# Kernel tuning notes

Measured on AMD Instinct MI355X. Metric: run time of the kernel, lower is better.

## Reference

```python
import jax, jax.numpy as jnp
import numpy as np

B, T, I, H, N, M, O = 256, 128, 512, 512, 1024, 512, 512
EPS = 1e-8


def setup_inputs() -> dict:
    key = jax.random.key(0)
    ks = jax.random.split(key, 10)
    rn = lambda k, shape, s: jax.random.normal(k, shape, jnp.float32) * s
    s_h, s_i, s_m = 1.0 / np.sqrt(H), 1.0 / np.sqrt(I), 1.0 / np.sqrt(M)
    return {
        "x": jax.random.normal(ks[0], (B, T, 1, I), jnp.float32),
        "mem0": jnp.full((N, M), 1e-6, jnp.float32),          # memory init fill_(1e-6)
        "wr0": jnp.eye(B, N, dtype=jnp.float32),               # torch.eye(batch, N)
        "ww0": jnp.eye(B, N, dtype=jnp.float32),
        "h0": rn(ks[1], (B, H), 1.0 / H),                      # normal_(0, 1/num_hidden)
        "Wx": rn(ks[2], (I, H), s_i),
        "Wr": rn(ks[3], (M, H), s_m),
        "bh": jnp.zeros((H,), jnp.float32),
        "Whr": rn(ks[4], (H, M + 6), s_h),                      # read head: k,beta,g,s(3),gamma
        "bhr": jnp.zeros((M + 6,), jnp.float32),
        "Whw": rn(ks[5], (H, M + 6), s_h),                      # write head addressing
        "bhw": jnp.zeros((M + 6,), jnp.float32),
        "Wea": rn(ks[6], (H, 2 * M), s_h),                      # write head erase/add
        "bea": jnp.zeros((2 * M,), jnp.float32),
        "Wo": rn(ks[7], (H, O), s_h),
        "bo": jnp.zeros((O,), jnp.float32),
    }


def _address(h, w_prev, mem, Wh, bh_):
    # Standard NTM addressing: content -> interpolate -> shift -> sharpen.
    p = h @ Wh + bh_                                   # (B, M+6)
    k = jnp.tanh(p[:, :M])                             # key (B, M)
    beta = jax.nn.softplus(p[:, M:M + 1])              # strength >= 0
    g = jax.nn.sigmoid(p[:, M + 1:M + 2])              # gate in (0,1)
    s = jax.nn.softmax(p[:, M + 2:M + 5], axis=-1)     # shift over {-1,0,+1}
    gamma = 1.0 + jax.nn.softplus(p[:, M + 5:M + 6])   # sharpen >= 1
    kn = k / (jnp.linalg.norm(k, axis=-1, keepdims=True) + EPS)
    mn = mem / (jnp.linalg.norm(mem, axis=-1, keepdims=True) + EPS)
    wc = jax.nn.softmax(beta * (kn @ mn.T), axis=-1)   # content weights (B, N)
    wg = g * wc + (1.0 - g) * w_prev                   # interpolation (strictly > 0)
    wt = (s[:, 0:1] * jnp.roll(wg, -1, axis=1)
          + s[:, 1:2] * wg
          + s[:, 2:3] * jnp.roll(wg, 1, axis=1))       # circular shift conv
    wp = wt ** gamma
    return wp / (jnp.sum(wp, axis=-1, keepdims=True) + EPS)


def reference(x, mem0, wr0, ww0, h0, Wx, Wr, bh, Whr, bhr, Whw, bhw, Wea, bea, Wo, bo):
    xs = jnp.transpose(x[:, :, 0, :], (1, 0, 2))       # (T, B, I): x.permute(1,0,2,3)

    def step(carry, x_t):
        mem, wr, ww, h = carry
        # write head (get_weights=False): erase/add into memory with prev ww
        ea = h @ Wea + bea
        e = jax.nn.sigmoid(ea[:, :M])                  # (B, M)
        a = jnp.tanh(ea[:, M:])                        # (B, M)
        mem = (mem * (1.0 - jnp.einsum('bn,bm->nm', ww, e) / B)
               + jnp.einsum('bn,bm->nm', ww, a) / B)   # batch-averaged, mem shared (N, M)
        # read head (get_weights=False): r = wr @ M
        r = wr @ mem                                   # (B, M)
        # controller.step(x_t, r)
        h = jnp.tanh(x_t @ Wx + r @ Wr + bh)           # (B, H)
        # new addressing weights from updated hidden + updated memory
        ww = _address(h, ww, mem, Whw, bhw)
        wr = _address(h, wr, mem, Whr, bhr)
        out = jax.nn.sigmoid(h @ Wo + bo)              # (B, O)
        return (mem, wr, ww, h), out

    _, outs = jax.lax.scan(step, (mem0, wr0, ww0, h0), xs)  # outs (T, B, O)
    return jnp.transpose(outs, (1, 0, 2))              # (B, T, O)
```

## Files before the change

kernel.cpp:

```cpp
#include <hip/hip_runtime.h>
#include <math.h>

#define B_ 256
#define T_ 128
#define I_ 512
#define H_ 512
#define N_ 1024
#define M_ 512
#define O_ 512
#define EPS_ 1e-8f
#define NB_ 512

typedef unsigned short u16;
typedef unsigned long long u64;
typedef __attribute__((ext_vector_type(8))) short v8s;
typedef __attribute__((ext_vector_type(4))) float v4f;

#define MFMA(a, b, c) __builtin_amdgcn_mfma_f32_16x16x32_bf16(a, b, c, 0, 0, 0)

#define PL_BIG 1310720
#define PL_WXT 262144
#define PL_WRT 262144
#define PL_MEM 524288
#define PL_W   262144
#define PL_H   131072
#define PL_KH  262144

template <typename T>
__device__ __forceinline__ T lda_(const T* p) {
    return __hip_atomic_load(const_cast<T*>(p), __ATOMIC_RELAXED, __HIP_MEMORY_SCOPE_AGENT);
}
template <typename T>
__device__ __forceinline__ void sta_(T* p, T v) {
    __hip_atomic_store(p, v, __ATOMIC_RELAXED, __HIP_MEMORY_SCOPE_AGENT);
}
__device__ __forceinline__ uint4 ld16_(const u16* p) {
    const u64* q = (const u64*)p;
    u64 lo = __hip_atomic_load(const_cast<u64*>(q), __ATOMIC_RELAXED, __HIP_MEMORY_SCOPE_AGENT);
    u64 hi = __hip_atomic_load(const_cast<u64*>(q + 1), __ATOMIC_RELAXED, __HIP_MEMORY_SCOPE_AGENT);
    uint4 r;
    r.x = (unsigned)lo; r.y = (unsigned)(lo >> 32);
    r.z = (unsigned)hi; r.w = (unsigned)(hi >> 32);
    return r;
}
__device__ __forceinline__ void st64_(u16* p, u16 a, u16 b, u16 c, u16 d) {
    u64 v = (u64)a | ((u64)b << 16) | ((u64)c << 32) | ((u64)d << 48);
    __hip_atomic_store((u64*)p, v, __ATOMIC_RELAXED, __HIP_MEMORY_SCOPE_AGENT);
}

__device__ __forceinline__ float sigm_(float x) { return 1.f / (1.f + expf(-x)); }
__device__ __forceinline__ float softplus_(float x) { return x > 20.f ? x : log1pf(expf(x)); }
__device__ __forceinline__ u16 f2bf(float f) {
    unsigned u = __float_as_uint(f);
    u += 0x7fffu + ((u >> 16) & 1u);
    return (u16)(u >> 16);
}
__device__ __forceinline__ float bf2f(u16 h) { return __uint_as_float((unsigned)h << 16); }
__device__ __forceinline__ void split2(float f, u16& h, u16& m) {
    h = f2bf(f);
    m = f2bf(f - bf2f(h));
}

__device__ __forceinline__ float wave_sum_(float v) {
#pragma unroll
    for (int o = 32; o > 0; o >>= 1) v += __shfl_down(v, o);
    return v;
}
__device__ __forceinline__ float wave_max_(float v) {
#pragma unroll
    for (int o = 32; o > 0; o >>= 1) v = fmaxf(v, __shfl_down(v, o));
    return v;
}
__device__ float block_sum_(float v, float* s) {
    int lane = threadIdx.x & 63, wid = threadIdx.x >> 6, nw = blockDim.x >> 6;
    v = wave_sum_(v);
    if (lane == 0) s[wid] = v;
    __syncthreads();
    float r = (threadIdx.x < nw) ? s[threadIdx.x] : 0.f;
    if (wid == 0) { r = wave_sum_(r); if (lane == 0) s[0] = r; }
    __syncthreads();
    float out = s[0];
    __syncthreads();
    return out;
}
__device__ float block_max_(float v, float* s) {
    int lane = threadIdx.x & 63, wid = threadIdx.x >> 6, nw = blockDim.x >> 6;
    v = wave_max_(v);
    if (lane == 0) s[wid] = v;
    __syncthreads();
    float r = (threadIdx.x < nw) ? s[threadIdx.x] : -3.4e38f;
    if (wid == 0) { r = wave_max_(r); if (lane == 0) s[0] = r; }
    __syncthreads();
    float out = s[0];
    __syncthreads();
    return out;
}

__device__ __forceinline__ void gsync(unsigned* slots, unsigned* flag, unsigned epoch) {
    __syncthreads();
    if (threadIdx.x == 0)
        __hip_atomic_store(&slots[blockIdx.x * 16], epoch, __ATOMIC_RELAXED,
                           __HIP_MEMORY_SCOPE_AGENT);
    if (blockIdx.x == 0) {
        while (__hip_atomic_load(&slots[threadIdx.x * 16], __ATOMIC_RELAXED,
                                 __HIP_MEMORY_SCOPE_AGENT) < epoch)
            __builtin_amdgcn_s_sleep(1);
        while (__hip_atomic_load(&slots[(threadIdx.x + 256) * 16], __ATOMIC_RELAXED,
                                 __HIP_MEMORY_SCOPE_AGENT) < epoch)
            __builtin_amdgcn_s_sleep(1);
        __syncthreads();
        if (threadIdx.x == 0)
            __hip_atomic_store(flag, epoch, __ATOMIC_RELAXED, __HIP_MEMORY_SCOPE_AGENT);
    } else if (threadIdx.x == 0) {
        while (__hip_atomic_load(flag, __ATOMIC_RELAXED, __HIP_MEMORY_SCOPE_AGENT) < epoch)
            __builtin_amdgcn_s_sleep(1);
    }
    __syncthreads();
}

struct EpiEA0 {
    const float* bea; u16* eT; u16* aT;
    __device__ void operator()(int r0, int c, v4f v) const {
#pragma unroll
        for (int r = 0; r < 4; r++) {
            float val = v[r] + bea[c];
            u16* dst;
            int b = r0 + r;
            if (c < M_) { val = sigm_(val); dst = eT + (size_t)c * B_ + b; }
            else        { val = tanhf(val); dst = aT + (size_t)(c - M_) * B_ + b; }
            u16 h, m; split2(val, h, m);
            dst[0] = h; dst[PL_H] = m;
        }
    }
};
struct EpiR {
    u16* rp;
    __device__ void operator()(int r0, int c, v4f v) const {
#pragma unroll
        for (int r = 0; r < 4; r++) {
            u16 h, m; split2(v[r], h, m);
            size_t idx = (size_t)(r0 + r) * M_ + c;
            sta_(rp + idx, h); sta_(rp + PL_H + idx, m);
        }
    }
};
struct EpiH {
    const float* xwxt; const float* bh; float* hf; u16* hp;
    __device__ void operator()(int r0, int c, v4f v) const {
#pragma unroll
        for (int r = 0; r < 4; r++) {
            int b = r0 + r;
            float val = tanhf(v[r] + xwxt[(size_t)b * (T_ * O_) + c] + bh[c]);
            size_t idx = (size_t)b * H_ + c;
            sta_(hf + idx, val);
            u16 h, m; split2(val, h, m);
            sta_(hp + idx, h); sta_(hp + PL_H + idx, m);
        }
    }
};
struct EpiFused {
    const float* bhw; const float* bhr; const float* bo; const float* bea;
    u16* khp; float* outt; u16* eT; u16* aT;
    __device__ void operator()(int r0, int c, v4f v) const {
        if (c < 1024) {
            int head = c >> 9, key = c & 511;
            const float* bb = head ? bhr : bhw;
#pragma unroll
            for (int r = 0; r < 4; r++) {
                float val = tanhf(v[r] + bb[key]);
                size_t idx = (size_t)(head * 256 + r0 + r) * M_ + key;
                u16 h, m; split2(val, h, m);
                sta_(khp + idx, h); sta_(khp + PL_KH + idx, m);
            }
        } else if (c < 1536) {
            int o = c - 1024;
#pragma unroll
            for (int r = 0; r < 4; r++)
                outt[(size_t)(r0 + r) * (T_ * O_) + o] = sigm_(v[r] + bo[o]);
        } else {
            int m = c - 1536;
#pragma unroll
            for (int r = 0; r < 4; r++) {
                float val = v[r] + bea[m];
                u16* dst;
                int b = r0 + r;
                if (m < M_) { val = sigm_(val); dst = eT + (size_t)m * B_ + b; }
                else        { val = tanhf(val); dst = aT + (size_t)(m - M_) * B_ + b; }
                u16 h, mm; split2(val, h, mm);
                sta_(dst, h); sta_(dst + PL_H, mm);
            }
        }
    }
};

struct NtmArgs {
    const u16 *BigT, *WxT, *WrT;
    u16 *mem_pl, *memT_pl, *wwT_pl, *wr_pl, *h_pl, *r_pl, *eT_pl, *aT_pl, *kh_pl;
    float *memf, *wwf, *wrf, *hf, *logits, *ssqp;
    const float *w6w, *w6r, *bh, *bhw, *bhr, *bea, *bo;
    float* out;
    unsigned* slots;
    unsigned* flag;
};

template <bool AS, bool BS, class Epi>
__device__ __forceinline__ void dev_gemm32(char* smc, const u16* __restrict__ Ap, int lda, int apl,
                                           const u16* __restrict__ Bp, int ldb, int bpl,
                                           int K, int row0, int col0, const Epi& epi) {
    typedef u16 (*AsT)[32][40];
    typedef u16 (*BsT)[64][40];
    AsT As = (AsT)smc;
    BsT Bs = (BsT)(smc + 5120);
    const int tid = threadIdx.x, lane = tid & 63, w = tid >> 6;
    const int wy = w >> 1, wx = w & 1, q = lane >> 4, l15 = lane & 15;
    uint4 ra, rb[2];
    auto loadA = [&](int k0) {
        int s = tid, p = s >> 7, rr = (s >> 2) & 31, kg = s & 3;
        const u16* ap = Ap + (size_t)p * apl + (size_t)(row0 + rr) * lda + k0 + kg * 8;
        ra = AS ? ld16_(ap) : *(const uint4*)ap;
    };
    auto loadB = [&](int k0) {
#pragma unroll
        for (int j = 0; j < 2; j++) {
            int s = j * 256 + tid, p = s >> 8, rr = (s >> 2) & 63, kg = s & 3;
            const u16* bp = Bp + (size_t)p * bpl + (size_t)(col0 + rr) * ldb + k0 + kg * 8;
            rb[j] = BS ? ld16_(bp) : *(const uint4*)bp;
        }
    };
    v4f acc[2] = {};
    loadA(0); loadB(0);
    for (int k0 = 0; k0 < K; k0 += 32) {
        {
            int s = tid, p = s >> 7, rr = (s >> 2) & 31, kg = s & 3;
            *(uint4*)&As[p][rr][kg * 8] = ra;
        }
#pragma unroll
        for (int j = 0; j < 2; j++) {
            int s = j * 256 + tid, p = s >> 8, rr = (s >> 2) & 63, kg = s & 3;
            *(uint4*)&Bs[p][rr][kg * 8] = rb[j];
        }
        __syncthreads();
        if (k0 + 32 < K) { loadA(k0 + 32); loadB(k0 + 32); }
        v8s af0 = *(const v8s*)&As[0][wy * 16 + l15][q * 8];
        v8s af1 = *(const v8s*)&As[1][wy * 16 + l15][q * 8];
        v8s bf[2][2];
#pragma unroll
        for (int nt = 0; nt < 2; nt++) {
            bf[nt][0] = *(const v8s*)&Bs[0][wx * 32 + nt * 16 + l15][q * 8];
            bf[nt][1] = *(const v8s*)&Bs[1][wx * 32 + nt * 16 + l15][q * 8];
        }
#pragma unroll
        for (int nt = 0; nt < 2; nt++) {
            v4f c = acc[nt];
            c = MFMA(af0, bf[nt][0], c);
            c = MFMA(af0, bf[nt][1], c);
            c = MFMA(af1, bf[nt][0], c);
            acc[nt] = c;
        }
        __syncthreads();
    }
#pragma unroll
    for (int nt = 0; nt < 2; nt++)
        epi(row0 + wy * 16 + q * 4, col0 + wx * 32 + nt * 16 + l15, acc[nt]);
}

template <bool AS, bool BS, class Epi>
__device__ __forceinline__ void dev_gemm64(char* smc, const u16* __restrict__ Ap, int lda, int apl,
                                           const u16* __restrict__ Bp, int ldb, int bpl,
                                           int K, int row0, int col0, const Epi& epi) {
    typedef u16 (*T64)[64][40];
    T64 As = (T64)smc;
    T64 Bs = (T64)(smc + 10240);
    const int tid = threadIdx.x, lane = tid & 63, w = tid >> 6;
    const int wy = w >> 1, wx = w & 1, q = lane >> 4, l15 = lane & 15;
    uint4 ra[2], rb[2];
    auto loadAll = [&](int k0) {
#pragma unroll
        for (int j = 0; j < 2; j++) {
            int s = j * 256 + tid, p = s >> 8, rr = (s >> 2) & 63, kg = s & 3;
            const u16* ap = Ap + (size_t)p * apl + (size_t)(row0 + rr) * lda + k0 + kg * 8;
            const u16* bp = Bp + (size_t)p * bpl + (size_t)(col0 + rr) * ldb + k0 + kg * 8;
            ra[j] = AS ? ld16_(ap) : *(const uint4*)ap;
            rb[j] = BS ? ld16_(bp) : *(const uint4*)bp;
        }
    };
    v4f acc[2][2] = {};
    loadAll(0);
    for (int k0 = 0; k0 < K; k0 += 32) {
#pragma unroll
        for (int j = 0; j < 2; j++) {
            int s = j * 256 + tid, p = s >> 8, rr = (s >> 2) & 63, kg = s & 3;
            *(uint4*)&As[p][rr][kg * 8] = ra[j];
            *(uint4*)&Bs[p][rr][kg * 8] = rb[j];
        }
        __syncthreads();
        if (k0 + 32 < K) loadAll(k0 + 32);
        v8s af[2][2], bf[2][2];
#pragma unroll
        for (int mt = 0; mt < 2; mt++) {
            af[mt][0] = *(const v8s*)&As[0][wy * 32 + mt * 16 + l15][q * 8];
            af[mt][1] = *(const v8s*)&As[1][wy * 32 + mt * 16 + l15][q * 8];
            bf[mt][0] = *(const v8s*)&Bs[0][wx * 32 + mt * 16 + l15][q * 8];
            bf[mt][1] = *(const v8s*)&Bs[1][wx * 32 + mt * 16 + l15][q * 8];
        }
#pragma unroll
        for (int mt = 0; mt < 2; mt++)
#pragma unroll
            for (int nt = 0; nt < 2; nt++) {
                v4f c = acc[mt][nt];
                c = MFMA(af[mt][0], bf[nt][0], c);
                c = MFMA(af[mt][0], bf[nt][1], c);
                c = MFMA(af[mt][1], bf[nt][0], c);
                acc[mt][nt] = c;
            }
        __syncthreads();
    }
#pragma unroll
    for (int mt = 0; mt < 2; mt++)
#pragma unroll
        for (int nt = 0; nt < 2; nt++)
            epi(row0 + wy * 32 + mt * 16 + q * 4, col0 + wx * 32 + nt * 16 + l15, acc[mt][nt]);
}

__device__ void dev_memupd(char* smc, int bid, const NtmArgs& A) {
    typedef u16 (*T64)[64][40];
    T64 As = (T64)smc;
    T64 Be = (T64)(smc + 10240);
    T64 Ba = (T64)(smc + 20480);
    float* ssqs = (float*)(smc + 30720);
    const int tid = threadIdx.x, lane = tid & 63, w = tid >> 6;
    const int wy = w >> 1, wx = w & 1, q = lane >> 4, l15 = lane & 15;
    const int bx = bid & 7, by = bid >> 3;
    const int row0 = by * 64, col0 = bx * 64;
    if (tid < 64) ssqs[tid] = 0.f;
    uint4 rA[2], rE[2], rB[2];
    auto loadAll = [&](int k0) {
#pragma unroll
        for (int j = 0; j < 2; j++) {
            int s = j * 256 + tid, p = s >> 8, rr = (s >> 2) & 63, kg = s & 3;
            rA[j] = ld16_(A.wwT_pl + (size_t)p * PL_W + (size_t)(row0 + rr) * B_ + k0 + kg * 8);
            rE[j] = ld16_(A.eT_pl + (size_t)p * PL_H + (size_t)(col0 + rr) * B_ + k0 + kg * 8);
            rB[j] = ld16_(A.aT_pl + (size_t)p * PL_H + (size_t)(col0 + rr) * B_ + k0 + kg * 8);
        }
    };
    v4f ae[2][2] = {}, aa[2][2] = {};
    loadAll(0);
    for (int k0 = 0; k0 < B_; k0 += 32) {
#pragma unroll
        for (int j = 0; j < 2; j++) {
            int s = j * 256 + tid, p = s >> 8, rr = (s >> 2) & 63, kg = s & 3;
            *(uint4*)&As[p][rr][kg * 8] = rA[j];
            *(uint4*)&Be[p][rr][kg * 8] = rE[j];
            *(uint4*)&Ba[p][rr][kg * 8] = rB[j];
        }
        __syncthreads();
        if (k0 + 32 < B_) loadAll(k0 + 32);
        v8s af[2][2], be[2][2], ba[2][2];
#pragma unroll
        for (int mt = 0; mt < 2; mt++) {
            af[mt][0] = *(const v8s*)&As[0][wy * 32 + mt * 16 + l15][q * 8];
            af[mt][1] = *(const v8s*)&As[1][wy * 32 + mt * 16 + l15][q * 8];
            be[mt][0] = *(const v8s*)&Be[0][wx * 32 + mt * 16 + l15][q * 8];
            be[mt][1] = *(const v8s*)&Be[1][wx * 32 + mt * 16 + l15][q * 8];
            ba[mt][0] = *(const v8s*)&Ba[0][wx * 32 + mt * 16 + l15][q * 8];
            ba[mt][1] = *(const v8s*)&Ba[1][wx * 32 + mt * 16 + l15][q * 8];
        }
#pragma unroll
        for (int mt = 0; mt < 2; mt++)
#pragma unroll
            for (int nt = 0; nt < 2; nt++) {
                v4f c = ae[mt][nt];
                c = MFMA(af[mt][0], be[nt][0], c);
                c = MFMA(af[mt][0], be[nt][1], c);
                c = MFMA(af[mt][1], be[nt][0], c);
                ae[mt][nt] = c;
                v4f d = aa[mt][nt];
                d = MFMA(af[mt][0], ba[nt][0], d);
                d = MFMA(af[mt][0], ba[nt][1], d);
                d = MFMA(af[mt][1], ba[nt][0], d);
                aa[mt][nt] = d;
            }
        __syncthreads();
    }
    const float invB = 1.f / (float)B_;
#pragma unroll
    for (int mt = 0; mt < 2; mt++)
#pragma unroll
        for (int nt = 0; nt < 2; nt++) {
            int r0 = row0 + wy * 32 + mt * 16 + q * 4;
            int c  = col0 + wx * 32 + nt * 16 + l15;
            u16 hv[4][2];
#pragma unroll
            for (int r = 0; r < 4; r++) {
                size_t idx = (size_t)(r0 + r) * M_ + c;
                float old = A.memf[idx];
                float nv = old * (1.f - ae[mt][nt][r] * invB) + aa[mt][nt][r] * invB;
                A.memf[idx] = nv;
                u16 h, m; split2(nv, h, m);
                sta_(A.mem_pl + idx, h); sta_(A.mem_pl + PL_MEM + idx, m);
                hv[r][0] = h; hv[r][1] = m;
                atomicAdd(&ssqs[r0 + r - row0], nv * nv);
            }
            size_t tb = (size_t)c * N_ + r0;
            st64_(A.memT_pl + tb, hv[0][0], hv[1][0], hv[2][0], hv[3][0]);
            st64_(A.memT_pl + PL_MEM + tb, hv[0][1], hv[1][1], hv[2][1], hv[3][1]);
        }
    __syncthreads();
    if (tid < 64) sta_(A.ssqp + (size_t)(row0 + tid) * 8 + bx, ssqs[tid]);
}

__device__ void dev_logits(char* smc, int bx, int by, const NtmArgs& A) {
    typedef u16 (*T64)[64][40];
    T64 As = (T64)smc;
    T64 Bs = (T64)(smc + 10240);
    float* invn_s = (float*)(smc + 20480);
    const int tid = threadIdx.x, lane = tid & 63, w = tid >> 6;
    const int wy = w >> 1, wx = w & 1, q = lane >> 4, l15 = lane & 15;
    const int row0 = by * 64, col0 = bx * 64;
    if (tid < 64) {
        float s = 0.f;
#pragma unroll
        for (int j = 0; j < 8; j++) s += lda_(A.ssqp + (size_t)(col0 + tid) * 8 + j);
        invn_s[tid] = 1.f / (sqrtf(s) + EPS_);
    }
    uint4 ra[2], rb[2];
    auto loadAll = [&](int k0) {
#pragma unroll
        for (int j = 0; j < 2; j++) {
            int s = j * 256 + tid, p = s >> 8, rr = (s >> 2) & 63, kg = s & 3;
            ra[j] = ld16_(A.kh_pl + (size_t)p * PL_KH + (size_t)(row0 + rr) * M_ + k0 + kg * 8);
            rb[j] = ld16_(A.mem_pl + (size_t)p * PL_MEM + (size_t)(col0 + rr) * M_ + k0 + kg * 8);
        }
    };
    v4f acc[2][2] = {};
    loadAll(0);
    for (int k0 = 0; k0 < M_; k0 += 32) {
#pragma unroll
        for (int j = 0; j < 2; j++) {
            int s = j * 256 + tid, p = s >> 8, rr = (s >> 2) & 63, kg = s & 3;
            *(uint4*)&As[p][rr][kg * 8] = ra[j];
            *(uint4*)&Bs[p][rr][kg * 8] = rb[j];
        }
        __syncthreads();
        if (k0 + 32 < M_) loadAll(k0 + 32);
        v8s af[2][2], bf[2][2];
#pragma unroll
        for (int mt = 0; mt < 2; mt++) {
            af[mt][0] = *(const v8s*)&As[0][wy * 32 + mt * 16 + l15][q * 8];
            af[mt][1] = *(const v8s*)&As[1][wy * 32 + mt * 16 + l15][q * 8];
            bf[mt][0] = *(const v8s*)&Bs[0][wx * 32 + mt * 16 + l15][q * 8];
            bf[mt][1] = *(const v8s*)&Bs[1][wx * 32 + mt * 16 + l15][q * 8];
        }
#pragma unroll
        for (int mt = 0; mt < 2; mt++)
#pragma unroll
            for (int nt = 0; nt < 2; nt++) {
                v4f c = acc[mt][nt];
                c = MFMA(af[mt][0], bf[nt][0], c);
                c = MFMA(af[mt][0], bf[nt][1], c);
                c = MFMA(af[mt][1], bf[nt][0], c);
                acc[mt][nt] = c;
            }
        __syncthreads();
    }
#pragma unroll
    for (int mt = 0; mt < 2; mt++)
#pragma unroll
        for (int nt = 0; nt < 2; nt++) {
            int r0 = row0 + wy * 32 + mt * 16 + q * 4;
            int c  = col0 + wx * 32 + nt * 16 + l15;
            float in_ = invn_s[c - col0];
#pragma unroll
            for (int r = 0; r < 4; r++)
                sta_(A.logits + (size_t)(r0 + r) * N_ + c, acc[mt][nt][r] * in_);
        }
}

__device__ void dev_addr(char* smc, int row, const NtmArgs& A) {
    float* wgs = (float*)smc;
    float* red = (float*)(smc + 4096);
    int head = row >> 8, b = row & 255;
    const float* w6 = head ? A.w6r : A.w6w;
    const float* bias = head ? A.bhr : A.bhw;
    float* wf = head ? A.wrf : A.wwf;
    int tid = threadIdx.x;
    float d0 = 0, d1 = 0, d2 = 0, d3 = 0, d4 = 0, d5 = 0, ssq = 0;
#pragma unroll
    for (int j = 0; j < 2; j++) {
        int k = tid + j * 256;
        float hv = lda_(A.hf + (size_t)b * H_ + k);
        const float* wk = w6 + k * 6;
        d0 += hv * wk[0]; d1 += hv * wk[1]; d2 += hv * wk[2];
        d3 += hv * wk[3]; d4 += hv * wk[4]; d5 += hv * wk[5];
        size_t ki = (size_t)row * M_ + k;
        float kv = bf2f(lda_(A.kh_pl + ki)) + bf2f(lda_(A.kh_pl + PL_KH + ki));
        ssq += kv * kv;
    }
    d0 = block_sum_(d0, red); d1 = block_sum_(d1, red); d2 = block_sum_(d2, red);
    d3 = block_sum_(d3, red); d4 = block_sum_(d4, red); d5 = block_sum_(d5, red);
    ssq = block_sum_(ssq, red);
    float beta = softplus_(d0 + bias[M_]);
    float g = sigm_(d1 + bias[M_ + 1]);
    float a0 = d2 + bias[M_ + 2], a1 = d3 + bias[M_ + 3], a2 = d4 + bias[M_ + 4];
    float mx3 = fmaxf(a0, fmaxf(a1, a2));
    float e0 = expf(a0 - mx3), e1 = expf(a1 - mx3), e2 = expf(a2 - mx3);
    float es = e0 + e1 + e2;
    float s0 = e0 / es, s1 = e1 / es, s2 = e2 / es;
    float gamma = 1.f + softplus_(d5 + bias[M_ + 5]);
    float rowsc = beta / (sqrtf(ssq) + EPS_);
    const u64* lp = (const u64*)(A.logits + (size_t)row * N_ + tid * 4);
    u64 la = lda_(lp), lb = lda_(lp + 1);
    float l[4];
    l[0] = __uint_as_float((unsigned)la) * rowsc;
    l[1] = __uint_as_float((unsigned)(la >> 32)) * rowsc;
    l[2] = __uint_as_float((unsigned)lb) * rowsc;
    l[3] = __uint_as_float((unsigned)(lb >> 32)) * rowsc;
    float mx = fmaxf(fmaxf(l[0], l[1]), fmaxf(l[2], l[3]));
    mx = block_max_(mx, red);
    float ex[4], sum = 0.f;
#pragma unroll
    for (int j = 0; j < 4; j++) { ex[j] = expf(l[j] - mx); sum += ex[j]; }
    sum = block_sum_(sum, red);
    float inv = 1.f / sum;
    float wprev[4];
#pragma unroll
    for (int j = 0; j < 4; j++) wprev[j] = wf[(size_t)b * N_ + tid * 4 + j];
#pragma unroll
    for (int j = 0; j < 4; j++) wgs[tid * 4 + j] = g * ex[j] * inv + (1.f - g) * wprev[j];
    __syncthreads();
    float wp[4], psum = 0.f;
#pragma unroll
    for (int j = 0; j < 4; j++) {
        int n = tid * 4 + j;
        float wt = s0 * wgs[(n + 1) & (N_ - 1)] + s1 * wgs[n] + s2 * wgs[(n - 1) & (N_ - 1)];
        float v = expf(gamma * logf(wt));
        wp[j] = v; psum += v;
    }
    psum = block_sum_(psum, red);
    float invp = 1.f / (psum + EPS_);
#pragma unroll
    for (int j = 0; j < 4; j++) {
        int n = tid * 4 + j;
        float val = wp[j] * invp;
        wf[(size_t)b * N_ + n] = val;
        u16 h, m; split2(val, h, m);
        if (head == 0) {
            size_t tb = (size_t)n * B_ + b;
            sta_(A.wwT_pl + tb, h); sta_(A.wwT_pl + PL_W + tb, m);
        } else {
            size_t idx = (size_t)b * N_ + n;
            sta_(A.wr_pl + idx, h); sta_(A.wr_pl + PL_W + idx, m);
        }
    }
}

__global__ __launch_bounds__(256, 2) void ntm_loop(NtmArgs A) {
    __shared__ __align__(16) char sm[31232];
    const int bid = blockIdx.x;
    unsigned ep = 0;
    for (int t = 0; t < T_; t++) {
        if (bid < 128) dev_memupd(sm, bid, A);
        gsync(A.slots, A.flag, ++ep);
        if (bid < 32) {
            int bx = bid & 7, by = bid >> 3;
            dev_gemm64<true, true>(sm, A.wr_pl, 1024, PL_W, A.memT_pl, 1024, PL_MEM, 1024,
                                   by * 64, bx * 64, EpiR{A.r_pl});
        }
        gsync(A.slots, A.flag, ++ep);
        if (bid < 32) {
            int bx = bid & 7, by = bid >> 3;
            dev_gemm64<true, false>(sm, A.r_pl, 512, PL_H, A.WrT, 512, PL_WRT, 512,
                                    by * 64, bx * 64,
                                    EpiH{A.out + (size_t)t * O_, A.bh, A.hf, A.h_pl});
        }
        gsync(A.slots, A.flag, ++ep);
        if (bid < 320) {
            int g = bid & 7, idx = bid >> 3;
            int bx = g * 5 + idx % 5, by = idx / 5;
            dev_gemm32<true, false>(sm, A.h_pl, 512, PL_H, A.BigT, 512, PL_BIG, 512,
                                    by * 32, bx * 64,
                                    EpiFused{A.bhw, A.bhr, A.bo, A.bea, A.kh_pl,
                                             A.out + (size_t)t * O_, A.eT_pl, A.aT_pl});
        }
        gsync(A.slots, A.flag, ++ep);
        if (bid < 128) {
            int g = bid & 7, idx = bid >> 3;
            int bx = g * 2 + (idx & 1), by = idx >> 1;
            dev_logits(sm, bx, by, A);
        }
        gsync(A.slots, A.flag, ++ep);
        for (int row = bid; row < 2 * B_; row += NB_) dev_addr(sm, row, A);
        gsync(A.slots, A.flag, ++ep);
    }
}

template <int TM, class Epi>
__global__ __launch_bounds__(256) void gemm2(const u16* __restrict__ Ap, int lda, int apl,
                                             const u16* __restrict__ Bp, int ldb, int bpl,
                                             int K, Epi epi) {
    constexpr int AL = (TM * 32 * 2) / (256 * 8);
    constexpr int MT = TM / 32;
    __shared__ u16 As[2][TM][40];
    __shared__ u16 Bs[2][64][40];
    const int tid = threadIdx.x, lane = tid & 63, w = tid >> 6;
    const int wy = w >> 1, wx = w & 1, q = lane >> 4, l15 = lane & 15;
    const int row0 = blockIdx.y * TM, col0 = blockIdx.x * 64;
    uint4 ra[AL], rb[2];
    auto loadA = [&](int k0) {
#pragma unroll
        for (int j = 0; j < AL; j++) {
            int s = j * 256 + tid, p = s / (TM * 4), rr = (s >> 2) % TM, kg = s & 3;
            ra[j] = *(const uint4*)(Ap + (size_t)p * apl + (size_t)(row0 + rr) * lda + k0 + kg * 8);
        }
    };
    auto loadB = [&](int k0) {
#pragma unroll
        for (int j = 0; j < 2; j++) {
            int s = j * 256 + tid, p = s >> 8, rr = (s >> 2) & 63, kg = s & 3;
            rb[j] = *(const uint4*)(Bp + (size_t)p * bpl + (size_t)(col0 + rr) * ldb + k0 + kg * 8);
        }
    };
    v4f acc[MT][2] = {};
    loadA(0); loadB(0);
    for (int k0 = 0; k0 < K; k0 += 32) {
#pragma unroll
        for (int j = 0; j < AL; j++) {
            int s = j * 256 + tid, p = s / (TM * 4), rr = (s >> 2) % TM, kg = s & 3;
            *(uint4*)&As[p][rr][kg * 8] = ra[j];
        }
#pragma unroll
        for (int j = 0; j < 2; j++) {
            int s = j * 256 + tid, p = s >> 8, rr = (s >> 2) & 63, kg = s & 3;
            *(uint4*)&Bs[p][rr][kg * 8] = rb[j];
        }
        __syncthreads();
        if (k0 + 32 < K) { loadA(k0 + 32); loadB(k0 + 32); }
        v8s af[MT][2], bf[2][2];
#pragma unroll
        for (int mt = 0; mt < MT; mt++) {
            af[mt][0] = *(const v8s*)&As[0][wy * (TM / 2) + mt * 16 + l15][q * 8];
            af[mt][1] = *(const v8s*)&As[1][wy * (TM / 2) + mt * 16 + l15][q * 8];
        }
#pragma unroll
        for (int nt = 0; nt < 2; nt++) {
            bf[nt][0] = *(const v8s*)&Bs[0][wx * 32 + nt * 16 + l15][q * 8];
            bf[nt][1] = *(const v8s*)&Bs[1][wx * 32 + nt * 16 + l15][q * 8];
        }
#pragma unroll
        for (int mt = 0; mt < MT; mt++)
#pragma unroll
            for (int nt = 0; nt < 2; nt++) {
                v4f c = acc[mt][nt];
                c = MFMA(af[mt][0], bf[nt][0], c);
                c = MFMA(af[mt][0], bf[nt][1], c);
                c = MFMA(af[mt][1], bf[nt][0], c);
                acc[mt][nt] = c;
            }
        __syncthreads();
    }
#pragma unroll
    for (int mt = 0; mt < MT; mt++)
#pragma unroll
        for (int nt = 0; nt < 2; nt++)
            epi(row0 + wy * (TM / 2) + mt * 16 + q * 4, col0 + wx * 32 + nt * 16 + l15, acc[mt][nt]);
}

__global__ __launch_bounds__(256) void gemm2_xwx(const float* __restrict__ x, const u16* __restrict__ WxT,
                                                 float* __restrict__ outbuf) {
    __shared__ u16 As[2][64][40];
    __shared__ u16 Bs[2][64][40];
    const int tid = threadIdx.x, lane = tid & 63, w = tid >> 6;
    const int wy = w >> 1, wx = w & 1, q = lane >> 4, l15 = lane & 15;
    const int row0 = blockIdx.y * 64, col0 = blockIdx.x * 64;
    const int sr = tid >> 2, ss = (tid & 3) * 8;
    const int arow = row0 + sr, ab = arow & 255, at = arow >> 8;
    const float* Asrc = x + ((size_t)ab * T_ + at) * I_ + ss;
    v4f acc[2][2] = {};
    for (int k0 = 0; k0 < I_; k0 += 32) {
        float4 f0 = *(const float4*)(Asrc + k0);
        float4 f1 = *(const float4*)(Asrc + k0 + 4);
        float av8[8] = {f0.x, f0.y, f0.z, f0.w, f1.x, f1.y, f1.z, f1.w};
#pragma unroll
        for (int j = 0; j < 8; j++) {
            u16 h, m; split2(av8[j], h, m);
            As[0][sr][ss + j] = h; As[1][sr][ss + j] = m;
        }
#pragma unroll
        for (int p = 0; p < 2; p++)
            *(uint4*)&Bs[p][sr][ss] = *(const uint4*)&WxT[(size_t)p * PL_WXT + (size_t)(col0 + sr) * I_ + k0 + ss];
        __syncthreads();
        v8s af[2][2], bf[2][2];
#pragma unroll
        for (int mt = 0; mt < 2; mt++) {
            af[mt][0] = *(const v8s*)&As[0][wy * 32 + mt * 16 + l15][q * 8];
            af[mt][1] = *(const v8s*)&As[1][wy * 32 + mt * 16 + l15][q * 8];
            bf[mt][0] = *(const v8s*)&Bs[0][wx * 32 + mt * 16 + l15][q * 8];
            bf[mt][1] = *(const v8s*)&Bs[1][wx * 32 + mt * 16 + l15][q * 8];
        }
#pragma unroll
        for (int mt = 0; mt < 2; mt++)
#pragma unroll
            for (int nt = 0; nt < 2; nt++) {
                v4f c = acc[mt][nt];
                c = MFMA(af[mt][0], bf[nt][0], c);
                c = MFMA(af[mt][0], bf[nt][1], c);
                c = MFMA(af[mt][1], bf[nt][0], c);
                acc[mt][nt] = c;
            }
        __syncthreads();
    }
#pragma unroll
    for (int mt = 0; mt < 2; mt++)
#pragma unroll
        for (int nt = 0; nt < 2; nt++) {
            int r0 = row0 + wy * 32 + mt * 16 + q * 4;
            int c  = col0 + wx * 32 + nt * 16 + l15;
#pragma unroll
            for (int r = 0; r < 4; r++) {
                int row = r0 + r, b = row & 255, t = row >> 8;
                outbuf[((size_t)b * T_ + t) * O_ + c] = acc[mt][nt][r];
            }
        }
}

__global__ __launch_bounds__(256) void decomp_t(const float* __restrict__ in, int ldin, int c0,
                                                int R, u16* __restrict__ outp, int opl) {
    __shared__ float Ls[32][33];
    const int r0 = blockIdx.x * 32, cB = blockIdx.y * 32;
    const int tid = threadIdx.x;
    int lr = tid >> 3, lc = (tid & 7) * 4;
#pragma unroll
    for (int j = 0; j < 4; j++)
        Ls[lr][lc + j] = in[(size_t)(r0 + lr) * ldin + c0 + cB + lc + j];
    __syncthreads();
    int lc2 = tid >> 3, lr2 = (tid & 7) * 4;
    u16 hv[4], mv[4];
#pragma unroll
    for (int j = 0; j < 4; j++) split2(Ls[lr2 + j][lc2], hv[j], mv[j]);
    size_t base = (size_t)(cB + lc2) * R + r0 + lr2;
    *(ushort4*)&outp[0 * (size_t)opl + base] = make_ushort4(hv[0], hv[1], hv[2], hv[3]);
    *(ushort4*)&outp[1 * (size_t)opl + base] = make_ushort4(mv[0], mv[1], mv[2], mv[3]);
}

__global__ __launch_bounds__(512) void wh6_kernel(const float* __restrict__ Whw, const float* __restrict__ Whr,
                                                  float* __restrict__ w6w, float* __restrict__ w6r,
                                                  unsigned* __restrict__ barz) {
    int k = threadIdx.x;
    if (blockIdx.x == 0) {
        for (int i = k; i < NB_ * 16 + 16; i += 512) barz[i] = 0u;
    }
    const float* src = blockIdx.x ? Whr : Whw;
    float* dst = blockIdx.x ? w6r : w6w;
#pragma unroll
    for (int j = 0; j < 6; j++) dst[k * 6 + j] = src[(size_t)k * (M_ + 6) + M_ + j];
}
__global__ __launch_bounds__(256) void init_mem(const float* __restrict__ mem0, float* __restrict__ memf,
                                                u16* __restrict__ mem_pl, u16* __restrict__ memT_pl) {
    int n = blockIdx.x;
    for (int c = threadIdx.x; c < M_; c += 256) {
        float v = mem0[(size_t)n * M_ + c];
        size_t idx = (size_t)n * M_ + c;
        memf[idx] = v;
        u16 h, m; split2(v, h, m);
        mem_pl[idx] = h; mem_pl[PL_MEM + idx] = m;
        size_t tb = (size_t)c * N_ + n;
        memT_pl[tb] = h; memT_pl[PL_MEM + tb] = m;
    }
}
__global__ __launch_bounds__(256) void init_w(const float* __restrict__ wr0, const float* __restrict__ ww0,
                                              float* __restrict__ wrf, float* __restrict__ wwf,
                                              u16* __restrict__ wr_pl, u16* __restrict__ wwT_pl) {
    int b = blockIdx.x;
    for (int n = threadIdx.x; n < N_; n += 256) {
        size_t idx = (size_t)b * N_ + n;
        float vw = ww0[idx]; wwf[idx] = vw;
        u16 h, m; split2(vw, h, m);
        size_t tb = (size_t)n * B_ + b;
        wwT_pl[tb] = h; wwT_pl[PL_W + tb] = m;
        float vr = wr0[idx]; wrf[idx] = vr;
        split2(vr, h, m);
        wr_pl[idx] = h; wr_pl[PL_W + idx] = m;
    }
}
__global__ __launch_bounds__(64) void init_h(const float* __restrict__ h0, float* __restrict__ hf,
                                             u16* __restrict__ hp) {
    int b = blockIdx.x;
    for (int c = threadIdx.x; c < H_; c += 64) {
        size_t idx = (size_t)b * H_ + c;
        float v = h0[idx];
        hf[idx] = v;
        u16 h, m; split2(v, h, m);
        hp[idx] = h; hp[PL_H + idx] = m;
    }
}

extern "C" void kernel_launch(void* const* d_in, const int* in_sizes, int n_in,
                              void* d_out, int out_size, void* d_ws, size_t ws_size,
                              hipStream_t stream) {
    (void)in_sizes; (void)n_in; (void)out_size; (void)ws_size;
    const float* x    = (const float*)d_in[0];
    const float* mem0 = (const float*)d_in[1];
    const float* wr0  = (const float*)d_in[2];
    const float* ww0  = (const float*)d_in[3];
    const float* h0   = (const float*)d_in[4];
    const float* Wx   = (const float*)d_in[5];
    const float* Wr   = (const float*)d_in[6];
    const float* bh   = (const float*)d_in[7];
    const float* Whr  = (const float*)d_in[8];
    const float* bhr  = (const float*)d_in[9];
    const float* Whw  = (const float*)d_in[10];
    const float* bhw  = (const float*)d_in[11];
    const float* Wea  = (const float*)d_in[12];
    const float* bea  = (const float*)d_in[13];
    const float* Wo   = (const float*)d_in[14];
    const float* bo   = (const float*)d_in[15];
    float* out = (float*)d_out;

    char* wsb = (char*)d_ws;
    size_t off = 0;
    auto carveU = [&](size_t elems) { u16* p = (u16*)(wsb + off); off += elems * sizeof(u16); return p; };
    u16* BigT    = carveU(2 * (size_t)PL_BIG);
    u16* WxT     = carveU(2 * (size_t)PL_WXT);
    u16* WrT     = carveU(2 * (size_t)PL_WRT);
    u16* mem_pl  = carveU(2 * (size_t)PL_MEM);
    u16* memT_pl = carveU(2 * (size_t)PL_MEM);
    u16* wwT_pl  = carveU(2 * (size_t)PL_W);
    u16* wr_pl   = carveU(2 * (size_t)PL_W);
    u16* h_pl    = carveU(2 * (size_t)PL_H);
    u16* r_pl    = carveU(2 * (size_t)PL_H);
    u16* eT_pl   = carveU(2 * (size_t)PL_H);
    u16* aT_pl   = carveU(2 * (size_t)PL_H);
    u16* kh_pl   = carveU(2 * (size_t)PL_KH);
    auto carveF = [&](size_t elems) { float* p = (float*)(wsb + off); off += elems * sizeof(float); return p; };
    float* memf   = carveF((size_t)N_ * M_);
    float* wwf    = carveF((size_t)B_ * N_);
    float* wrf    = carveF((size_t)B_ * N_);
    float* hf     = carveF((size_t)B_ * H_);
    float* logits = carveF((size_t)2 * B_ * N_);
    float* ssqp   = carveF((size_t)N_ * 8);
    float* w6w    = carveF(H_ * 6);
    float* w6r    = carveF(H_ * 6);
    off = (off + 127) & ~(size_t)127;
    unsigned* slots = (unsigned*)(wsb + off);
    unsigned* flag  = slots + NB_ * 16;
    off += (NB_ * 16 + 16) * sizeof(unsigned) + 64;

    decomp_t<<<dim3(16, 16), 256, 0, stream>>>(Whw, M_ + 6, 0, 512, BigT, PL_BIG);
    decomp_t<<<dim3(16, 16), 256, 0, stream>>>(Whr, M_ + 6, 0, 512, BigT + (size_t)512 * 512, PL_BIG);
    decomp_t<<<dim3(16, 16), 256, 0, stream>>>(Wo, 512, 0, 512, BigT + (size_t)1024 * 512, PL_BIG);
    decomp_t<<<dim3(16, 32), 256, 0, stream>>>(Wea, 1024, 0, 512, BigT + (size_t)1536 * 512, PL_BIG);
    decomp_t<<<dim3(16, 16), 256, 0, stream>>>(Wx, 512, 0, 512, WxT, PL_WXT);
    decomp_t<<<dim3(16, 16), 256, 0, stream>>>(Wr, 512, 0, 512, WrT, PL_WRT);
    wh6_kernel<<<2, 512, 0, stream>>>(Whw, Whr, w6w, w6r, slots);
    init_mem<<<N_, 256, 0, stream>>>(mem0, memf, mem_pl, memT_pl);
    init_w<<<B_, 256, 0, stream>>>(wr0, ww0, wrf, wwf, wr_pl, wwT_pl);
    init_h<<<B_, 64, 0, stream>>>(h0, hf, h_pl);
    gemm2_xwx<<<dim3(8, 512), 256, 0, stream>>>(x, WxT, out);
    gemm2<32, EpiEA0><<<dim3(16, 8), 256, 0, stream>>>(
        h_pl, 512, PL_H, BigT + (size_t)1536 * 512, 512, PL_BIG, 512, EpiEA0{bea, eT_pl, aT_pl});

    NtmArgs A;
    A.BigT = BigT; A.WxT = WxT; A.WrT = WrT;
    A.mem_pl = mem_pl; A.memT_pl = memT_pl; A.wwT_pl = wwT_pl; A.wr_pl = wr_pl;
    A.h_pl = h_pl; A.r_pl = r_pl; A.eT_pl = eT_pl; A.aT_pl = aT_pl; A.kh_pl = kh_pl;
    A.memf = memf; A.wwf = wwf; A.wrf = wrf; A.hf = hf; A.logits = logits; A.ssqp = ssqp;
    A.w6w = w6w; A.w6r = w6r; A.bh = bh; A.bhw = bhw; A.bhr = bhr; A.bea = bea; A.bo = bo;
    A.out = out;
    A.slots = slots;
    A.flag = flag;
    ntm_loop<<<dim3(NB_), dim3(256), 0, stream>>>(A);
}
```

Measured before the change: 17.16 ms.

## Interleave bf16 hi/lo split planes into packed 32-bit words

Result: faster. 15.99 ms (-6.8%).

```diff
diff --git a/kernel.cpp b/kernel.cpp
--- a/kernel.cpp
+++ b/kernel.cpp
@@ -12,20 +12,13 @@
 #define NB_ 512
 
 typedef unsigned short u16;
+typedef unsigned u32;
 typedef unsigned long long u64;
 typedef __attribute__((ext_vector_type(8))) short v8s;
 typedef __attribute__((ext_vector_type(4))) float v4f;
 
 #define MFMA(a, b, c) __builtin_amdgcn_mfma_f32_16x16x32_bf16(a, b, c, 0, 0, 0)
 
-#define PL_BIG 1310720
-#define PL_WXT 262144
-#define PL_WRT 262144
-#define PL_MEM 524288
-#define PL_W   262144
-#define PL_H   131072
-#define PL_KH  262144
-
 template <typename T>
 __device__ __forceinline__ T lda_(const T* p) {
     return __hip_atomic_load(const_cast<T*>(p), __ATOMIC_RELAXED, __HIP_MEMORY_SCOPE_AGENT);
@@ -34,18 +27,13 @@
 __device__ __forceinline__ void sta_(T* p, T v) {
     __hip_atomic_store(p, v, __ATOMIC_RELAXED, __HIP_MEMORY_SCOPE_AGENT);
 }
-__device__ __forceinline__ uint4 ld16_(const u16* p) {
-    const u64* q = (const u64*)p;
-    u64 lo = __hip_atomic_load(const_cast<u64*>(q), __ATOMIC_RELAXED, __HIP_MEMORY_SCOPE_AGENT);
-    u64 hi = __hip_atomic_load(const_cast<u64*>(q + 1), __ATOMIC_RELAXED, __HIP_MEMORY_SCOPE_AGENT);
+__device__ __forceinline__ uint4 ld16_(const u32* p) {
+    u64 lo = lda_((const u64*)p);
+    u64 hi = lda_((const u64*)p + 1);
     uint4 r;
-    r.x = (unsigned)lo; r.y = (unsigned)(lo >> 32);
-    r.z = (unsigned)hi; r.w = (unsigned)(hi >> 32);
+    r.x = (u32)lo; r.y = (u32)(lo >> 32);
+    r.z = (u32)hi; r.w = (u32)(hi >> 32);
     return r;
-}
-__device__ __forceinline__ void st64_(u16* p, u16 a, u16 b, u16 c, u16 d) {
-    u64 v = (u64)a | ((u64)b << 16) | ((u64)c << 32) | ((u64)d << 48);
-    __hip_atomic_store((u64*)p, v, __ATOMIC_RELAXED, __HIP_MEMORY_SCOPE_AGENT);
 }
 
 __device__ __forceinline__ float sigm_(float x) { return 1.f / (1.f + expf(-x)); }
@@ -59,6 +47,16 @@
 __device__ __forceinline__ void split2(float f, u16& h, u16& m) {
     h = f2bf(f);
     m = f2bf(f - bf2f(h));
+}
+__device__ __forceinline__ u32 pack2_(float f) {
+    u16 h, m; split2(f, h, m);
+    return (u32)h | ((u32)m << 16);
+}
+__device__ __forceinline__ void deint_(uint4 r, u32* hi, u32* lo) {
+    hi[0] = (r.x & 0xffffu) | (r.y << 16);
+    hi[1] = (r.z & 0xffffu) | (r.w << 16);
+    lo[0] = (r.x >> 16) | (r.y & 0xffff0000u);
+    lo[1] = (r.z >> 16) | (r.w & 0xffff0000u);
 }
 
 __device__ __forceinline__ float wave_sum_(float v) {
@@ -119,48 +117,41 @@
 }
 
 struct EpiEA0 {
-    const float* bea; u16* eT; u16* aT;
+    const float* bea; u32* eT; u32* aT;
     __device__ void operator()(int r0, int c, v4f v) const {
 #pragma unroll
         for (int r = 0; r < 4; r++) {
             float val = v[r] + bea[c];
-            u16* dst;
+            u32* dst;
             int b = r0 + r;
             if (c < M_) { val = sigm_(val); dst = eT + (size_t)c * B_ + b; }
             else        { val = tanhf(val); dst = aT + (size_t)(c - M_) * B_ + b; }
-            u16 h, m; split2(val, h, m);
-            dst[0] = h; dst[PL_H] = m;
+            dst[0] = pack2_(val);
         }
     }
 };
 struct EpiR {
-    u16* rp;
+    u32* rp;
     __device__ void operator()(int r0, int c, v4f v) const {
 #pragma unroll
-        for (int r = 0; r < 4; r++) {
-            u16 h, m; split2(v[r], h, m);
-            size_t idx = (size_t)(r0 + r) * M_ + c;
-            sta_(rp + idx, h); sta_(rp + PL_H + idx, m);
-        }
+        for (int r = 0; r < 4; r++)
+            sta_(rp + (size_t)(r0 + r) * M_ + c, pack2_(v[r]));
     }
 };
 struct EpiH {
-    const float* xwxt; const float* bh; float* hf; u16* hp;
+    const float* xwxt; const float* bh; u32* hp;
     __device__ void operator()(int r0, int c, v4f v) const {
 #pragma unroll
         for (int r = 0; r < 4; r++) {
             int b = r0 + r;
             float val = tanhf(v[r] + xwxt[(size_t)b * (T_ * O_) + c] + bh[c]);
-            size_t idx = (size_t)b * H_ + c;
-            sta_(hf + idx, val);
-            u16 h, m; split2(val, h, m);
-            sta_(hp + idx, h); sta_(hp + PL_H + idx, m);
+            sta_(hp + (size_t)b * H_ + c, pack2_(val));
         }
     }
 };
 struct EpiFused {
     const float* bhw; const float* bhr; const float* bo; const float* bea;
-    u16* khp; float* outt; u16* eT; u16* aT;
+    u32* khp; float* outt; u32* eT; u32* aT;
     __device__ void operator()(int r0, int c, v4f v) const {
         if (c < 1024) {
             int head = c >> 9, key = c & 511;
@@ -168,9 +159,7 @@
 #pragma unroll
             for (int r = 0; r < 4; r++) {
                 float val = tanhf(v[r] + bb[key]);
-                size_t idx = (size_t)(head * 256 + r0 + r) * M_ + key;
-                u16 h, m; split2(val, h, m);
-                sta_(khp + idx, h); sta_(khp + PL_KH + idx, m);
+                sta_(khp + (size_t)(head * 256 + r0 + r) * M_ + key, pack2_(val));
             }
         } else if (c < 1536) {
             int o = c - 1024;
@@ -182,21 +171,20 @@
 #pragma unroll
             for (int r = 0; r < 4; r++) {
                 float val = v[r] + bea[m];
-                u16* dst;
+                u32* dst;
                 int b = r0 + r;
                 if (m < M_) { val = sigm_(val); dst = eT + (size_t)m * B_ + b; }
                 else        { val = tanhf(val); dst = aT + (size_t)(m - M_) * B_ + b; }
-                u16 h, mm; split2(val, h, mm);
-                sta_(dst, h); sta_(dst + PL_H, mm);
+                sta_(dst, pack2_(val));
             }
         }
     }
 };
 
 struct NtmArgs {
-    const u16 *BigT, *WxT, *WrT;
-    u16 *mem_pl, *memT_pl, *wwT_pl, *wr_pl, *h_pl, *r_pl, *eT_pl, *aT_pl, *kh_pl;
-    float *memf, *wwf, *wrf, *hf, *logits, *ssqp;
+    const u32 *BigT, *WrT;
+    u32 *mem_i, *memT_i, *wwT_i, *wr_i, *h_i, *r_i, *eT_i, *aT_i, *kh_i;
+    float *memf, *wwf, *wrf, *logits, *ssqp;
     const float *w6w, *w6r, *bh, *bhw, *bhr, *bea, *bo;
     float* out;
     unsigned* slots;
@@ -204,26 +192,26 @@
 };
 
 template <bool AS, bool BS, class Epi>
-__device__ __forceinline__ void dev_gemm32(char* smc, const u16* __restrict__ Ap, int lda, int apl,
-                                           const u16* __restrict__ Bp, int ldb, int bpl,
+__device__ __forceinline__ void dev_gemm32(char* smc, const u32* __restrict__ Ap, int lda,
+                                           const u32* __restrict__ Bp, int ldb,
                                            int K, int row0, int col0, const Epi& epi) {
-    typedef u16 (*AsT)[32][40];
-    typedef u16 (*BsT)[64][40];
-    AsT As = (AsT)smc;
-    BsT Bs = (BsT)(smc + 5120);
+    typedef u16 (*T40A)[32][40];
+    typedef u16 (*T40B)[64][40];
+    T40A As = (T40A)smc;
+    T40B Bs = (T40B)(smc + 5120);
     const int tid = threadIdx.x, lane = tid & 63, w = tid >> 6;
     const int wy = w >> 1, wx = w & 1, q = lane >> 4, l15 = lane & 15;
     uint4 ra, rb[2];
     auto loadA = [&](int k0) {
-        int s = tid, p = s >> 7, rr = (s >> 2) & 31, kg = s & 3;
-        const u16* ap = Ap + (size_t)p * apl + (size_t)(row0 + rr) * lda + k0 + kg * 8;
+        int row = tid >> 3, c4 = (tid & 7) * 4;
+        const u32* ap = Ap + (size_t)(row0 + row) * lda + k0 + c4;
         ra = AS ? ld16_(ap) : *(const uint4*)ap;
     };
     auto loadB = [&](int k0) {
 #pragma unroll
         for (int j = 0; j < 2; j++) {
-            int s = j * 256 + tid, p = s >> 8, rr = (s >> 2) & 63, kg = s & 3;
-            const u16* bp = Bp + (size_t)p * bpl + (size_t)(col0 + rr) * ldb + k0 + kg * 8;
+            int s = j * 256 + tid, row = s >> 3, c4 = (s & 7) * 4;
+            const u32* bp = Bp + (size_t)(col0 + row) * ldb + k0 + c4;
             rb[j] = BS ? ld16_(bp) : *(const uint4*)bp;
         }
     };
@@ -231,13 +219,17 @@
     loadA(0); loadB(0);
     for (int k0 = 0; k0 < K; k0 += 32) {
         {
-            int s = tid, p = s >> 7, rr = (s >> 2) & 31, kg = s & 3;
-            *(uint4*)&As[p][rr][kg * 8] = ra;
+            int row = tid >> 3, c4 = (tid & 7) * 4;
+            u32 hi[2], lo[2]; deint_(ra, hi, lo);
+            *(uint2*)&As[0][row][c4] = make_uint2(hi[0], hi[1]);
+            *(uint2*)&As[1][row][c4] = make_uint2(lo[0], lo[1]);
         }
 #pragma unroll
         for (int j = 0; j < 2; j++) {
-            int s = j * 256 + tid, p = s >> 8, rr = (s >> 2) & 63, kg = s & 3;
-            *(uint4*)&Bs[p][rr][kg * 8] = rb[j];
+            int s = j * 256 + tid, row = s >> 3, c4 = (s & 7) * 4;
+            u32 hi[2], lo[2]; deint_(rb[j], hi, lo);
+            *(uint2*)&Bs[0][row][c4] = make_uint2(hi[0], hi[1]);
+            *(uint2*)&Bs[1][row][c4] = make_uint2(lo[0], lo[1]);
         }
         __syncthreads();
         if (k0 + 32 < K) { loadA(k0 + 32); loadB(k0 + 32); }
@@ -265,8 +257,8 @@
 }
 
 template <bool AS, bool BS, class Epi>
-__device__ __forceinline__ void dev_gemm64(char* smc, const u16* __restrict__ Ap, int lda, int apl,
-                                           const u16* __restrict__ Bp, int ldb, int bpl,
+__device__ __forceinline__ void dev_gemm64(char* smc, const u32* __restrict__ Ap, int lda,
+                                           const u32* __restrict__ Bp, int ldb,
                                            int K, int row0, int col0, const Epi& epi) {
     typedef u16 (*T64)[64][40];
     T64 As = (T64)smc;
@@ -277,9 +269,9 @@
     auto loadAll = [&](int k0) {
 #pragma unroll
         for (int j = 0; j < 2; j++) {
-            int s = j * 256 + tid, p = s >> 8, rr = (s >> 2) & 63, kg = s & 3;
-            const u16* ap = Ap + (size_t)p * apl + (size_t)(row0 + rr) * lda + k0 + kg * 8;
-            const u16* bp = Bp + (size_t)p * bpl + (size_t)(col0 + rr) * ldb + k0 + kg * 8;
+            int s = j * 256 + tid, row = s >> 3, c4 = (s & 7) * 4;
+            const u32* ap = Ap + (size_t)(row0 + row) * lda + k0 + c4;
+            const u32* bp = Bp + (size_t)(col0 + row) * ldb + k0 + c4;
             ra[j] = AS ? ld16_(ap) : *(const uint4*)ap;
             rb[j] = BS ? ld16_(bp) : *(const uint4*)bp;
         }
@@ -289,9 +281,14 @@
     for (int k0 = 0; k0 < K; k0 += 32) {
 #pragma unroll
         for (int j = 0; j < 2; j++) {
-            int s = j * 256 + tid, p = s >> 8, rr = (s >> 2) & 63, kg = s & 3;
-            *(uint4*)&As[p][rr][kg * 8] = ra[j];
-            *(uint4*)&Bs[p][rr][kg * 8] = rb[j];
+            int s = j * 256 + tid, row = s >> 3, c4 = (s & 7) * 4;
+            u32 hi[2], lo[2];
+            deint_(ra[j], hi, lo);
+            *(uint2*)&As[0][row][c4] = make_uint2(hi[0], hi[1]);
+            *(uint2*)&As[1][row][c4] = make_uint2(lo[0], lo[1]);
+            deint_(rb[j], hi, lo);
+            *(uint2*)&Bs[0][row][c4] = make_uint2(hi[0], hi[1]);
+            *(uint2*)&Bs[1][row][c4] = make_uint2(lo[0], lo[1]);
         }
         __syncthreads();
         if (k0 + 32 < K) loadAll(k0 + 32);
@@ -337,10 +334,10 @@
     auto loadAll = [&](int k0) {
 #pragma unroll
         for (int j = 0; j < 2; j++) {
-            int s = j * 256 + tid, p = s >> 8, rr = (s >> 2) & 63, kg = s & 3;
-            rA[j] = ld16_(A.wwT_pl + (size_t)p * PL_W + (size_t)(row0 + rr) * B_ + k0 + kg * 8);
-            rE[j] = ld16_(A.eT_pl + (size_t)p * PL_H + (size_t)(col0 + rr) * B_ + k0 + kg * 8);
-            rB[j] = ld16_(A.aT_pl + (size_t)p * PL_H + (size_t)(col0 + rr) * B_ + k0 + kg * 8);
+            int s = j * 256 + tid, row = s >> 3, c4 = (s & 7) * 4;
+            rA[j] = ld16_(A.wwT_i + (size_t)(row0 + row) * B_ + k0 + c4);
+            rE[j] = ld16_(A.eT_i + (size_t)(col0 + row) * B_ + k0 + c4);
+            rB[j] = ld16_(A.aT_i + (size_t)(col0 + row) * B_ + k0 + c4);
         }
     };
     v4f ae[2][2] = {}, aa[2][2] = {};
@@ -348,10 +345,17 @@
     for (int k0 = 0; k0 < B_; k0 += 32) {
 #pragma unroll
         for (int j = 0; j < 2; j++) {
-            int s = j * 256 + tid, p = s >> 8, rr = (s >> 2) & 63, kg = s & 3;
-            *(uint4*)&As[p][rr][kg * 8] = rA[j];
-            *(uint4*)&Be[p][rr][kg * 8] = rE[j];
-            *(uint4*)&Ba[p][rr][kg * 8] = rB[j];
+            int s = j * 256 + tid, row = s >> 3, c4 = (s & 7) * 4;
+            u32 hi[2], lo[2];
+            deint_(rA[j], hi, lo);
+            *(uint2*)&As[0][row][c4] = make_uint2(hi[0], hi[1]);
+            *(uint2*)&As[1][row][c4] = make_uint2(lo[0], lo[1]);
+            deint_(rE[j], hi, lo);
+            *(uint2*)&Be[0][row][c4] = make_uint2(hi[0], hi[1]);
+            *(uint2*)&Be[1][row][c4] = make_uint2(lo[0], lo[1]);
+            deint_(rB[j], hi, lo);
+            *(uint2*)&Ba[0][row][c4] = make_uint2(hi[0], hi[1]);
+            *(uint2*)&Ba[1][row][c4] = make_uint2(lo[0], lo[1]);
         }
         __syncthreads();
         if (k0 + 32 < B_) loadAll(k0 + 32);
@@ -389,21 +393,21 @@
         for (int nt = 0; nt < 2; nt++) {
             int r0 = row0 + wy * 32 + mt * 16 + q * 4;
             int c  = col0 + wx * 32 + nt * 16 + l15;
-            u16 hv[4][2];
+            u32 pv4[4];
 #pragma unroll
             for (int r = 0; r < 4; r++) {
                 size_t idx = (size_t)(r0 + r) * M_ + c;
                 float old = A.memf[idx];
                 float nv = old * (1.f - ae[mt][nt][r] * invB) + aa[mt][nt][r] * invB;
                 A.memf[idx] = nv;
-                u16 h, m; split2(nv, h, m);
-                sta_(A.mem_pl + idx, h); sta_(A.mem_pl + PL_MEM + idx, m);
-                hv[r][0] = h; hv[r][1] = m;
+                u32 pv = pack2_(nv);
+                sta_(A.mem_i + idx, pv);
+                pv4[r] = pv;
                 atomicAdd(&ssqs[r0 + r - row0], nv * nv);
             }
             size_t tb = (size_t)c * N_ + r0;
-            st64_(A.memT_pl + tb, hv[0][0], hv[1][0], hv[2][0], hv[3][0]);
-            st64_(A.memT_pl + PL_MEM + tb, hv[0][1], hv[1][1], hv[2][1], hv[3][1]);
+            sta_((u64*)(A.memT_i + tb), (u64)pv4[0] | ((u64)pv4[1] << 32));
+            sta_((u64*)(A.memT_i + tb) + 1, (u64)pv4[2] | ((u64)pv4[3] << 32));
         }
     __syncthreads();
     if (tid < 64) sta_(A.ssqp + (size_t)(row0 + tid) * 8 + bx, ssqs[tid]);
@@ -427,9 +431,9 @@
     auto loadAll = [&](int k0) {
 #pragma unroll
         for (int j = 0; j < 2; j++) {
-            int s = j * 256 + tid, p = s >> 8, rr = (s >> 2) & 63, kg = s & 3;
-            ra[j] = ld16_(A.kh_pl + (size_t)p * PL_KH + (size_t)(row0 + rr) * M_ + k0 + kg * 8);
-            rb[j] = ld16_(A.mem_pl + (size_t)p * PL_MEM + (size_t)(col0 + rr) * M_ + k0 + kg * 8);
+            int s = j * 256 + tid, row = s >> 3, c4 = (s & 7) * 4;
+            ra[j] = ld16_(A.kh_i + (size_t)(row0 + row) * M_ + k0 + c4);
+            rb[j] = ld16_(A.mem_i + (size_t)(col0 + row) * M_ + k0 + c4);
         }
     };
     v4f acc[2][2] = {};
@@ -437,9 +441,14 @@
     for (int k0 = 0; k0 < M_; k0 += 32) {
 #pragma unroll
         for (int j = 0; j < 2; j++) {
-            int s = j * 256 + tid, p = s >> 8, rr = (s >> 2) & 63, kg = s & 3;
-            *(uint4*)&As[p][rr][kg * 8] = ra[j];
-            *(uint4*)&Bs[p][rr][kg * 8] = rb[j];
+            int s = j * 256 + tid, row = s >> 3, c4 = (s & 7) * 4;
+            u32 hi[2], lo[2];
+            deint_(ra[j], hi, lo);
+            *(uint2*)&As[0][row][c4] = make_uint2(hi[0], hi[1]);
+            *(uint2*)&As[1][row][c4] = make_uint2(lo[0], lo[1]);
+            deint_(rb[j], hi, lo);
+            *(uint2*)&Bs[0][row][c4] = make_uint2(hi[0], hi[1]);
+            *(uint2*)&Bs[1][row][c4] = make_uint2(lo[0], lo[1]);
         }
         __syncthreads();
         if (k0 + 32 < M_) loadAll(k0 + 32);
@@ -488,12 +497,13 @@
 #pragma unroll
     for (int j = 0; j < 2; j++) {
         int k = tid + j * 256;
-        float hv = lda_(A.hf + (size_t)b * H_ + k);
+        u32 hv2 = lda_(A.h_i + (size_t)b * H_ + k);
+        float hv = bf2f((u16)hv2) + bf2f((u16)(hv2 >> 16));
         const float* wk = w6 + k * 6;
         d0 += hv * wk[0]; d1 += hv * wk[1]; d2 += hv * wk[2];
         d3 += hv * wk[3]; d4 += hv * wk[4]; d5 += hv * wk[5];
-        size_t ki = (size_t)row * M_ + k;
-        float kv = bf2f(lda_(A.kh_pl + ki)) + bf2f(lda_(A.kh_pl + PL_KH + ki));
+        u32 kv2 = lda_(A.kh_i + (size_t)row * M_ + k);
+        float kv = bf2f((u16)kv2) + bf2f((u16)(kv2 >> 16));
         ssq += kv * kv;
     }
     d0 = block_sum_(d0, red); d1 = block_sum_(d1, red); d2 = block_sum_(d2, red);
@@ -511,10 +521,10 @@
     const u64* lp = (const u64*)(A.logits + (size_t)row * N_ + tid * 4);
     u64 la = lda_(lp), lb = lda_(lp + 1);
     float l[4];
-    l[0] = __uint_as_float((unsigned)la) * rowsc;
-    l[1] = __uint_as_float((unsigned)(la >> 32)) * rowsc;
-    l[2] = __uint_as_float((unsigned)lb) * rowsc;
-    l[3] = __uint_as_float((unsigned)(lb >> 32)) * rowsc;
+    l[0] = __uint_as_float((u32)la) * rowsc;
+    l[1] = __uint_as_float((u32)(la >> 32)) * rowsc;
+    l[2] = __uint_as_float((u32)lb) * rowsc;
+    l[3] = __uint_as_float((u32)(lb >> 32)) * rowsc;
     float mx = fmaxf(fmaxf(l[0], l[1]), fmaxf(l[2], l[3]));
     mx = block_max_(mx, red);
     float ex[4], sum = 0.f;
@@ -543,14 +553,9 @@
         int n = tid * 4 + j;
         float val = wp[j] * invp;
         wf[(size_t)b * N_ + n] = val;
-        u16 h, m; split2(val, h, m);
-        if (head == 0) {
-            size_t tb = (size_t)n * B_ + b;
-            sta_(A.wwT_pl + tb, h); sta_(A.wwT_pl + PL_W + tb, m);
-        } else {
-            size_t idx = (size_t)b * N_ + n;
-            sta_(A.wr_pl + idx, h); sta_(A.wr_pl + PL_W + idx, m);
-        }
+        u32 pv = pack2_(val);
+        if (head == 0) sta_(A.wwT_i + (size_t)n * B_ + b, pv);
+        else           sta_(A.wr_i + (size_t)b * N_ + n, pv);
     }
 }
 
@@ -563,24 +568,24 @@
         gsync(A.slots, A.flag, ++ep);
         if (bid < 32) {
             int bx = bid & 7, by = bid >> 3;
-            dev_gemm64<true, true>(sm, A.wr_pl, 1024, PL_W, A.memT_pl, 1024, PL_MEM, 1024,
-                                   by * 64, bx * 64, EpiR{A.r_pl});
+            dev_gemm64<true, true>(sm, A.wr_i, 1024, A.memT_i, 1024, 1024,
+                                   by * 64, bx * 64, EpiR{A.r_i});
         }
         gsync(A.slots, A.flag, ++ep);
         if (bid < 32) {
             int bx = bid & 7, by = bid >> 3;
-            dev_gemm64<true, false>(sm, A.r_pl, 512, PL_H, A.WrT, 512, PL_WRT, 512,
+            dev_gemm64<true, false>(sm, A.r_i, 512, A.WrT, 512, 512,
                                     by * 64, bx * 64,
-                                    EpiH{A.out + (size_t)t * O_, A.bh, A.hf, A.h_pl});
+                                    EpiH{A.out + (size_t)t * O_, A.bh, A.h_i});
         }
         gsync(A.slots, A.flag, ++ep);
         if (bid < 320) {
             int g = bid & 7, idx = bid >> 3;
             int bx = g * 5 + idx % 5, by = idx / 5;
-            dev_gemm32<true, false>(sm, A.h_pl, 512, PL_H, A.BigT, 512, PL_BIG, 512,
+            dev_gemm32<true, false>(sm, A.h_i, 512, A.BigT, 512, 512,
                                     by * 32, bx * 64,
-                                    EpiFused{A.bhw, A.bhr, A.bo, A.bea, A.kh_pl,
-                                             A.out + (size_t)t * O_, A.eT_pl, A.aT_pl});
+                                    EpiFused{A.bhw, A.bhr, A.bo, A.bea, A.kh_i,
+                                             A.out + (size_t)t * O_, A.eT_i, A.aT_i});
         }
         gsync(A.slots, A.flag, ++ep);
         if (bid < 128) {
@@ -594,78 +599,14 @@
     }
 }
 
-template <int TM, class Epi>
-__global__ __launch_bounds__(256) void gemm2(const u16* __restrict__ Ap, int lda, int apl,
-                                             const u16* __restrict__ Bp, int ldb, int bpl,
-                                             int K, Epi epi) {
-    constexpr int AL = (TM * 32 * 2) / (256 * 8);
-    constexpr int MT = TM / 32;
-    __shared__ u16 As[2][TM][40];
-    __shared__ u16 Bs[2][64][40];
-    const int tid = threadIdx.x, lane = tid & 63, w = tid >> 6;
-    const int wy = w >> 1, wx = w & 1, q = lane >> 4, l15 = lane & 15;
-    const int row0 = blockIdx.y * TM, col0 = blockIdx.x * 64;
-    uint4 ra[AL], rb[2];
-    auto loadA = [&](int k0) {
-#pragma unroll
-        for (int j = 0; j < AL; j++) {
-            int s = j * 256 + tid, p = s / (TM * 4), rr = (s >> 2) % TM, kg = s & 3;
-            ra[j] = *(const uint4*)(Ap + (size_t)p * apl + (size_t)(row0 + rr) * lda + k0 + kg * 8);
-        }
-    };
-    auto loadB = [&](int k0) {
-#pragma unroll
-        for (int j = 0; j < 2; j++) {
-            int s = j * 256 + tid, p = s >> 8, rr = (s >> 2) & 63, kg = s & 3;
-            rb[j] = *(const uint4*)(Bp + (size_t)p * bpl + (size_t)(col0 + rr) * ldb + k0 + kg * 8);
-        }
-    };
-    v4f acc[MT][2] = {};
-    loadA(0); loadB(0);
-    for (int k0 = 0; k0 < K; k0 += 32) {
-#pragma unroll
-        for (int j = 0; j < AL; j++) {
-            int s = j * 256 + tid, p = s / (TM * 4), rr = (s >> 2) % TM, kg = s & 3;
-            *(uint4*)&As[p][rr][kg * 8] = ra[j];
-        }
-#pragma unroll
-        for (int j = 0; j < 2; j++) {
-            int s = j * 256 + tid, p = s >> 8, rr = (s >> 2) & 63, kg = s & 3;
-            *(uint4*)&Bs[p][rr][kg * 8] = rb[j];
-        }
-        __syncthreads();
-        if (k0 + 32 < K) { loadA(k0 + 32); loadB(k0 + 32); }
-        v8s af[MT][2], bf[2][2];
-#pragma unroll
-        for (int mt = 0; mt < MT; mt++) {
-            af[mt][0] = *(const v8s*)&As[0][wy * (TM / 2) + mt * 16 + l15][q * 8];
-            af[mt][1] = *(const v8s*)&As[1][wy * (TM / 2) + mt * 16 + l15][q * 8];
-        }
-#pragma unroll
-        for (int nt = 0; nt < 2; nt++) {
-            bf[nt][0] = *(const v8s*)&Bs[0][wx * 32 + nt * 16 + l15][q * 8];
-            bf[nt][1] = *(const v8s*)&Bs[1][wx * 32 + nt * 16 + l15][q * 8];
-        }
-#pragma unroll
-        for (int mt = 0; mt < MT; mt++)
-#pragma unroll
-            for (int nt = 0; nt < 2; nt++) {
-                v4f c = acc[mt][nt];
-                c = MFMA(af[mt][0], bf[nt][0], c);
-                c = MFMA(af[mt][0], bf[nt][1], c);
-                c = MFMA(af[mt][1], bf[nt][0], c);
-                acc[mt][nt] = c;
-            }
-        __syncthreads();
-    }
-#pragma unroll
-    for (int mt = 0; mt < MT; mt++)
-#pragma unroll
-        for (int nt = 0; nt < 2; nt++)
-            epi(row0 + wy * (TM / 2) + mt * 16 + q * 4, col0 + wx * 32 + nt * 16 + l15, acc[mt][nt]);
-}
-
-__global__ __launch_bounds__(256) void gemm2_xwx(const float* __restrict__ x, const u16* __restrict__ WxT,
+__global__ __launch_bounds__(256) void gemm32_pro(const u32* __restrict__ Ap, int lda,
+                                                  const u32* __restrict__ Bp, int ldb,
+                                                  int K, EpiEA0 epi) {
+    __shared__ __align__(16) char sm[15616];
+    dev_gemm32<false, false>(sm, Ap, lda, Bp, ldb, K, blockIdx.y * 32, blockIdx.x * 64, epi);
+}
+
+__global__ __launch_bounds__(256) void gemm2_xwx(const float* __restrict__ x, const u32* __restrict__ WxT,
                                                  float* __restrict__ outbuf) {
     __shared__ u16 As[2][64][40];
     __shared__ u16 Bs[2][64][40];
@@ -686,8 +627,13 @@
             As[0][sr][ss + j] = h; As[1][sr][ss + j] = m;
         }
 #pragma unroll
-        for (int p = 0; p < 2; p++)
-            *(uint4*)&Bs[p][sr][ss] = *(const uint4*)&WxT[(size_t)p * PL_WXT + (size_t)(col0 + sr) * I_ + k0 + ss];
+        for (int j = 0; j < 2; j++) {
+            int s = j * 256 + tid, row = s >> 3, c4 = (s & 7) * 4;
+            uint4 rB = *(const uint4*)&WxT[(size_t)(col0 + row) * I_ + k0 + c4];
+            u32 hi[2], lo[2]; deint_(rB, hi, lo);
+            *(uint2*)&Bs[0][row][c4] = make_uint2(hi[0], hi[1]);
+            *(uint2*)&Bs[1][row][c4] = make_uint2(lo[0], lo[1]);
+        }
         __syncthreads();
         v8s af[2][2], bf[2][2];
 #pragma unroll
@@ -724,7 +670,7 @@
 }
 
 __global__ __launch_bounds__(256) void decomp_t(const float* __restrict__ in, int ldin, int c0,
-                                                int R, u16* __restrict__ outp, int opl) {
+                                                int R, u32* __restrict__ outp) {
     __shared__ float Ls[32][33];
     const int r0 = blockIdx.x * 32, cB = blockIdx.y * 32;
     const int tid = threadIdx.x;
@@ -734,12 +680,11 @@
         Ls[lr][lc + j] = in[(size_t)(r0 + lr) * ldin + c0 + cB + lc + j];
     __syncthreads();
     int lc2 = tid >> 3, lr2 = (tid & 7) * 4;
-    u16 hv[4], mv[4];
-#pragma unroll
-    for (int j = 0; j < 4; j++) split2(Ls[lr2 + j][lc2], hv[j], mv[j]);
+    u32 pv[4];
+#pragma unroll
+    for (int j = 0; j < 4; j++) pv[j] = pack2_(Ls[lr2 + j][lc2]);
     size_t base = (size_t)(cB + lc2) * R + r0 + lr2;
-    *(ushort4*)&outp[0 * (size_t)opl + base] = make_ushort4(hv[0], hv[1], hv[2], hv[3]);
-    *(ushort4*)&outp[1 * (size_t)opl + base] = make_ushort4(mv[0], mv[1], mv[2], mv[3]);
+    *(uint4*)&outp[base] = make_uint4(pv[0], pv[1], pv[2], pv[3]);
 }
 
 __global__ __launch_bounds__(512) void wh6_kernel(const float* __restrict__ Whw, const float* __restrict__ Whr,
@@ -755,43 +700,33 @@
     for (int j = 0; j < 6; j++) dst[k * 6 + j] = src[(size_t)k * (M_ + 6) + M_ + j];
 }
 __global__ __launch_bounds__(256) void init_mem(const float* __restrict__ mem0, float* __restrict__ memf,
-                                                u16* __restrict__ mem_pl, u16* __restrict__ memT_pl) {
+                                                u32* __restrict__ mem_i, u32* __restrict__ memT_i) {
     int n = blockIdx.x;
     for (int c = threadIdx.x; c < M_; c += 256) {
         float v = mem0[(size_t)n * M_ + c];
         size_t idx = (size_t)n * M_ + c;
         memf[idx] = v;
-        u16 h, m; split2(v, h, m);
-        mem_pl[idx] = h; mem_pl[PL_MEM + idx] = m;
-        size_t tb = (size_t)c * N_ + n;
-        memT_pl[tb] = h; memT_pl[PL_MEM + tb] = m;
+        u32 pv = pack2_(v);
+        mem_i[idx] = pv;
+        memT_i[(size_t)c * N_ + n] = pv;
     }
 }
 __global__ __launch_bounds__(256) void init_w(const float* __restrict__ wr0, const float* __restrict__ ww0,
                                               float* __restrict__ wrf, float* __restrict__ wwf,
-                                              u16* __restrict__ wr_pl, u16* __restrict__ wwT_pl) {
+                                              u32* __restrict__ wr_i, u32* __restrict__ wwT_i) {
     int b = blockIdx.x;
     for (int n = threadIdx.x; n < N_; n += 256) {
         size_t idx = (size_t)b * N_ + n;
         float vw = ww0[idx]; wwf[idx] = vw;
-        u16 h, m; split2(vw, h, m);
-        size_t tb = (size_t)n * B_ + b;
-        wwT_pl[tb] = h; wwT_pl[PL_W + tb] = m;
+        wwT_i[(size_t)n * B_ + b] = pack2_(vw);
         float vr = wr0[idx]; wrf[idx] = vr;
-        split2(vr, h, m);
-        wr_pl[idx] = h; wr_pl[PL_W + idx] = m;
-    }
-}
-__global__ __launch_bounds__(64) void init_h(const float* __restrict__ h0, float* __restrict__ hf,
-                                             u16* __restrict__ hp) {
+        wr_i[idx] = pack2_(vr);
+    }
+}
+__global__ __launch_bounds__(64) void init_h(const float* __restrict__ h0, u32* __restrict__ h_i) {
     int b = blockIdx.x;
-    for (int c = threadIdx.x; c < H_; c += 64) {
-        size_t idx = (size_t)b * H_ + c;
-        float v = h0[idx];
-        hf[idx] = v;
-        u16 h, m; split2(v, h, m);
-        hp[idx] = h; hp[PL_H + idx] = m;
-    }
+    for (int c = threadIdx.x; c < H_; c += 64)
+        h_i[(size_t)b * H_ + c] = pack2_(h0[(size_t)b * H_ + c]);
 }
 
 extern "C" void kernel_launch(void* const* d_in, const int* in_sizes, int n_in,
@@ -818,24 +753,23 @@
 
     char* wsb = (char*)d_ws;
     size_t off = 0;
-    auto carveU = [&](size_t elems) { u16* p = (u16*)(wsb + off); off += elems * sizeof(u16); return p; };
-    u16* BigT    = carveU(2 * (size_t)PL_BIG);
-    u16* WxT     = carveU(2 * (size_t)PL_WXT);
-    u16* WrT     = carveU(2 * (size_t)PL_WRT);
-    u16* mem_pl  = carveU(2 * (size_t)PL_MEM);
-    u16* memT_pl = carveU(2 * (size_t)PL_MEM);
-    u16* wwT_pl  = carveU(2 * (size_t)PL_W);
-    u16* wr_pl   = carveU(2 * (size_t)PL_W);
-    u16* h_pl    = carveU(2 * (size_t)PL_H);
-    u16* r_pl    = carveU(2 * (size_t)PL_H);
-    u16* eT_pl   = carveU(2 * (size_t)PL_H);
-    u16* aT_pl   = carveU(2 * (size_t)PL_H);
-    u16* kh_pl   = carveU(2 * (size_t)PL_KH);
+    auto carve32 = [&](size_t elems) { u32* p = (u32*)(wsb + off); off += elems * 4; return p; };
+    u32* BigT_i  = carve32((size_t)2560 * 512);
+    u32* WxT_i   = carve32((size_t)512 * 512);
+    u32* WrT_i   = carve32((size_t)512 * 512);
+    u32* mem_i   = carve32((size_t)1024 * 512);
+    u32* memT_i  = carve32((size_t)512 * 1024);
+    u32* wwT_i   = carve32((size_t)1024 * 256);
+    u32* wr_i    = carve32((size_t)256 * 1024);
+    u32* h_i     = carve32((size_t)256 * 512);
+    u32* r_i     = carve32((size_t)256 * 512);
+    u32* eT_i    = carve32((size_t)512 * 256);
+    u32* aT_i    = carve32((size_t)512 * 256);
+    u32* kh_i    = carve32((size_t)512 * 512);
     auto carveF = [&](size_t elems) { float* p = (float*)(wsb + off); off += elems * sizeof(float); return p; };
     float* memf   = carveF((size_t)N_ * M_);
     float* wwf    = carveF((size_t)B_ * N_);
     float* wrf    = carveF((size_t)B_ * N_);
-    float* hf     = carveF((size_t)B_ * H_);
     float* logits = carveF((size_t)2 * B_ * N_);
     float* ssqp   = carveF((size_t)N_ * 8);
     float* w6w    = carveF(H_ * 6);
@@ -845,25 +779,25 @@
     unsigned* flag  = slots + NB_ * 16;
     off += (NB_ * 16 + 16) * sizeof(unsigned) + 64;
 
-    decomp_t<<<dim3(16, 16), 256, 0, stream>>>(Whw, M_ + 6, 0, 512, BigT, PL_BIG);
-    decomp_t<<<dim3(16, 16), 256, 0, stream>>>(Whr, M_ + 6, 0, 512, BigT + (size_t)512 * 512, PL_BIG);
-    decomp_t<<<dim3(16, 16), 256, 0, stream>>>(Wo, 512, 0, 512, BigT + (size_t)1024 * 512, PL_BIG);
-    decomp_t<<<dim3(16, 32), 256, 0, stream>>>(Wea, 1024, 0, 512, BigT + (size_t)1536 * 512, PL_BIG);
-    decomp_t<<<dim3(16, 16), 256, 0, stream>>>(Wx, 512, 0, 512, WxT, PL_WXT);
-    decomp_t<<<dim3(16, 16), 256, 0, stream>>>(Wr, 512, 0, 512, WrT, PL_WRT);
+    decomp_t<<<dim3(16, 16), 256, 0, stream>>>(Whw, M_ + 6, 0, 512, BigT_i);
+    decomp_t<<<dim3(16, 16), 256, 0, stream>>>(Whr, M_ + 6, 0, 512, BigT_i + (size_t)512 * 512);
+    decomp_t<<<dim3(16, 16), 256, 0, stream>>>(Wo, 512, 0, 512, BigT_i + (size_t)1024 * 512);
+    decomp_t<<<dim3(16, 32), 256, 0, stream>>>(Wea, 1024, 0, 512, BigT_i + (size_t)1536 * 512);
+    decomp_t<<<dim3(16, 16), 256, 0, stream>>>(Wx, 512, 0, 512, WxT_i);
+    decomp_t<<<dim3(16, 16), 256, 0, stream>>>(Wr, 512, 0, 512, WrT_i);
     wh6_kernel<<<2, 512, 0, stream>>>(Whw, Whr, w6w, w6r, slots);
-    init_mem<<<N_, 256, 0, stream>>>(mem0, memf, mem_pl, memT_pl);
-    init_w<<<B_, 256, 0, stream>>>(wr0, ww0, wrf, wwf, wr_pl, wwT_pl);
-    init_h<<<B_, 64, 0, stream>>>(h0, hf, h_pl);
-    gemm2_xwx<<<dim3(8, 512), 256, 0, stream>>>(x, WxT, out);
-    gemm2<32, EpiEA0><<<dim3(16, 8), 256, 0, stream>>>(
-        h_pl, 512, PL_H, BigT + (size_t)1536 * 512, 512, PL_BIG, 512, EpiEA0{bea, eT_pl, aT_pl});
+    init_mem<<<N_, 256, 0, stream>>>(mem0, memf, mem_i, memT_i);
+    init_w<<<B_, 256, 0, stream>>>(wr0, ww0, wrf, wwf, wr_i, wwT_i);
+    init_h<<<B_, 64, 0, stream>>>(h0, h_i);
+    gemm2_xwx<<<dim3(8, 512), 256, 0, stream>>>(x, WxT_i, out);
+    gemm32_pro<<<dim3(16, 8), 256, 0, stream>>>(h_i, 512, BigT_i + (size_t)1536 * 512, 512, 512,
+                                                EpiEA0{bea, eT_i, aT_i});
 
     NtmArgs A;
-    A.BigT = BigT; A.WxT = WxT; A.WrT = WrT;
-    A.mem_pl = mem_pl; A.memT_pl = memT_pl; A.wwT_pl = wwT_pl; A.wr_pl = wr_pl;
-    A.h_pl = h_pl; A.r_pl = r_pl; A.eT_pl = eT_pl; A.aT_pl = aT_pl; A.kh_pl = kh_pl;
-    A.memf = memf; A.wwf = wwf; A.wrf = wrf; A.hf = hf; A.logits = logits; A.ssqp = ssqp;
+    A.BigT = BigT_i; A.WrT = WrT_i;
+    A.mem_i = mem_i; A.memT_i = memT_i; A.wwT_i = wwT_i; A.wr_i = wr_i;
+    A.h_i = h_i; A.r_i = r_i; A.eT_i = eT_i; A.aT_i = aT_i; A.kh_i = kh_i;
+    A.memf = memf; A.wwf = wwf; A.wrf = wrf; A.logits = logits; A.ssqp = ssqp;
     A.w6w = w6w; A.w6r = w6r; A.bh = bh; A.bhw = bhw; A.bhr = bhr; A.bea = bea; A.bo = bo;
     A.out = out;
     A.slots = slots;
```
